# Kernel optimization log

Measured on AMD Instinct MI355X. Metric: run time of the kernel, lower is better.

The kernel has to match this reference:

```python
import jax, jax.numpy as jnp
import numpy as np

B, S, D, H = 4, 2048, 1024, 16
HD = D // H  # head_dim = 64


def setup_inputs() -> dict:
    key = jax.random.key(0)
    ks = jax.random.split(key, 5)
    hidden_states = jax.random.normal(ks[0], (B, S, D), dtype=jnp.float32)
    # GPT-2 Conv1D: out = x @ W + b, W shape [in, out]
    w_attn = jax.random.normal(ks[1], (D, 3 * D), dtype=jnp.float32) * 0.02
    b_attn = jnp.zeros((3 * D,), dtype=jnp.float32)
    w_proj = jax.random.normal(ks[2], (D, D), dtype=jnp.float32) * 0.02
    b_proj = jnp.zeros((D,), dtype=jnp.float32)
    return {"hidden_states": hidden_states, "w_attn": w_attn, "b_attn": b_attn,
            "w_proj": w_proj, "b_proj": b_proj}


def reference(hidden_states, w_attn, b_attn, w_proj, b_proj):
    b, s, d = hidden_states.shape
    qkv = hidden_states @ w_attn + b_attn                     # [B,S,3D]
    q, k, v = jnp.split(qkv, 3, axis=-1)
    # split heads -> [B,H,S,HD]
    def heads(x):
        return x.reshape(b, s, H, HD).transpose(0, 2, 1, 3)
    q, k, v = heads(q), heads(k), heads(v)
    # scaled dot product; GPT-2 divides by sqrt(head_dim)
    scores = jnp.einsum("bhqd,bhkd->bhqk", q, k) / jnp.sqrt(jnp.float32(HD))
    causal = jnp.tril(jnp.ones((s, s), dtype=bool))           # [S,S]
    neg = jnp.finfo(scores.dtype).min
    scores = jnp.where(causal[None, None, :, :], scores, neg)
    attn = jax.nn.softmax(scores, axis=-1)
    ctx = jnp.einsum("bhqk,bhkd->bhqd", attn, v)              # [B,H,S,HD]
    ctx = ctx.transpose(0, 2, 1, 3).reshape(b, s, d)          # merge heads
    return ctx @ w_proj + b_proj
```

## Files before the change

kernel.cpp:

```cpp
#include <hip/hip_runtime.h>
#include <hip/hip_bf16.h>

typedef __bf16 bf16;
typedef bf16 bf16x8 __attribute__((ext_vector_type(8)));
typedef bf16 bf16x4 __attribute__((ext_vector_type(4)));
typedef float f32x4 __attribute__((ext_vector_type(4)));
typedef float f32x16 __attribute__((ext_vector_type(16)));
typedef unsigned int uint2v __attribute__((ext_vector_type(2)));

#define MFMA16(a, b, c) __builtin_amdgcn_mfma_f32_16x16x32_bf16(a, b, c, 0, 0, 0)
#define MFMA32(a, b, c) __builtin_amdgcn_mfma_f32_32x32x16_bf16(a, b, c, 0, 0, 0)

constexpr int Bn = 4, Sn = 2048, Dn = 1024, Hn = 16, HDn = 64;
constexpr int Mn = Bn * Sn;

__device__ __forceinline__ bf16x8 cvt8(float4 a, float4 b) {
  bf16x8 v = {(bf16)a.x, (bf16)a.y, (bf16)a.z, (bf16)a.w,
              (bf16)b.x, (bf16)b.y, (bf16)b.z, (bf16)b.w};
  return v;
}

__device__ __forceinline__ void load_lds16(const bf16* g, bf16* l) {
  __builtin_amdgcn_global_load_lds(
      (const __attribute__((address_space(1))) void*)g,
      (__attribute__((address_space(3))) void*)l, 16, 0, 0);
}

__device__ __forceinline__ unsigned cvt_pk_bf16(float lo, float hi) {
  unsigned r;
  asm("v_cvt_pk_bf16_f32 %0, %1, %2" : "=v"(r) : "v"(lo), "v"(hi));
  return r;
}

__global__ __launch_bounds__(256) void k_prep(const float* __restrict__ hidden,
                                              const float* __restrict__ w_attn,
                                              const float* __restrict__ w_proj,
                                              bf16* __restrict__ Xb,
                                              bf16* __restrict__ wattnT,
                                              bf16* __restrict__ wprojT) {
  __shared__ alignas(16) bf16 t[64][72];
  const int bx = blockIdx.x;
  const int tid = threadIdx.x;
  if (bx < 4096) {
    int i = bx * 256 + tid;
    const float4* p = (const float4*)hidden + (size_t)i * 2;
    float4 a = p[0], b = p[1];
    *((bf16x8*)Xb + i) = cvt8(a, b);
    return;
  }
  const float* in;
  bf16* out;
  int K = 1024, N, n0, k0;
  if (bx < 4864) {
    int idx = bx - 4096;
    in = w_attn; out = wattnT; N = 3072;
    n0 = (idx % 48) * 64; k0 = (idx / 48) * 64;
  } else {
    int idx = bx - 4864;
    in = w_proj; out = wprojT; N = 1024;
    n0 = (idx % 16) * 64; k0 = (idx / 16) * 64;
  }
  {
    int row = tid >> 2;
    int c16 = (tid & 3) * 16;
    const float* src = in + (size_t)(k0 + row) * N + n0 + c16;
    float4 f0 = ((const float4*)src)[0];
    float4 f1 = ((const float4*)src)[1];
    float4 f2 = ((const float4*)src)[2];
    float4 f3 = ((const float4*)src)[3];
    *(bf16x8*)&t[row][c16] = cvt8(f0, f1);
    *(bf16x8*)&t[row][c16 + 8] = cvt8(f2, f3);
  }
  __syncthreads();
#pragma unroll
  for (int i = 0; i < 2; i++) {
    int c = tid + i * 256;
    int nrow = c >> 3, kcol8 = (c & 7) * 8;
    bf16x8 v;
#pragma unroll
    for (int j = 0; j < 8; j++) v[j] = t[kcol8 + j][nrow];
    *(bf16x8*)(out + (size_t)(n0 + nrow) * K + k0 + kcol8) = v;
  }
}


__global__ __launch_bounds__(256) void k_gemm_qkv(const bf16* __restrict__ A,
                                                  const bf16* __restrict__ BT,
                                                  const float* __restrict__ bias,
                                                  bf16* __restrict__ Qo,
                                                  bf16* __restrict__ Ko,
                                                  bf16* __restrict__ Vt) {
  __shared__ alignas(16) bf16 la[128 * 32];
  __shared__ alignas(16) bf16 lb[128 * 32];
  const int tid = threadIdx.x;
  const int w = tid >> 6, lane = tid & 63, l15 = lane & 15, quad = lane >> 4;
  const int wm = w >> 1, wn = w & 1;
  const int bid = blockIdx.x;
  const int xcd = bid & 7, idx = bid >> 3;
  const int by = xcd * 8 + idx / 24;
  const int bx = idx % 24;
  const int m0 = by * 128, n0 = bx * 128;
  const int lrow = lane >> 2, lcol = (lane & 3) * 8;

  f32x4 acc[4][4];
#pragma unroll
  for (int i = 0; i < 4; i++)
#pragma unroll
    for (int j = 0; j < 4; j++) acc[i][j] = f32x4{0.f, 0.f, 0.f, 0.f};

  for (int k0 = 0; k0 < 1024; k0 += 32) {
    __syncthreads();
    load_lds16(A + (size_t)(m0 + w * 16 + lrow) * 1024 + k0 + lcol, &la[w * 512]);
    load_lds16(A + (size_t)(m0 + 64 + w * 16 + lrow) * 1024 + k0 + lcol, &la[(w + 4) * 512]);
    load_lds16(BT + (size_t)(n0 + w * 16 + lrow) * 1024 + k0 + lcol, &lb[w * 512]);
    load_lds16(BT + (size_t)(n0 + 64 + w * 16 + lrow) * 1024 + k0 + lcol, &lb[(w + 4) * 512]);
    __syncthreads();
    bf16x8 af[4], bfr[4];
#pragma unroll
    for (int i = 0; i < 4; i++)
      af[i] = *(const bf16x8*)&la[(wm * 64 + i * 16 + l15) * 32 + quad * 8];
#pragma unroll
    for (int j = 0; j < 4; j++)
      bfr[j] = *(const bf16x8*)&lb[(wn * 64 + j * 16 + l15) * 32 + quad * 8];
#pragma unroll
    for (int i = 0; i < 4; i++)
#pragma unroll
      for (int j = 0; j < 4; j++) acc[i][j] = MFMA16(af[i], bfr[j], acc[i][j]);
  }

#pragma unroll
  for (int j = 0; j < 4; j++) {
    int ng = n0 + wn * 64 + j * 16 + l15;
    float bs = bias[ng];
    int which = ng >> 10;
    int nloc = ng & 1023, hh = nloc >> 6, hd = nloc & 63;
#pragma unroll
    for (int i = 0; i < 4; i++) {
      int mg0 = m0 + wm * 64 + i * 16 + quad * 4;
      int bb = mg0 >> 11, ss = mg0 & 2047;
      if (which == 2) {
        bf16x4 v;
#pragma unroll
        for (int r = 0; r < 4; r++) v[r] = (bf16)(acc[i][j][r] + bs);
        *(bf16x4*)&Vt[((size_t)(bb * Hn + hh) * HDn + hd) * Sn + ss] = v;
      } else {
        bf16* dst = which ? Ko : Qo;
#pragma unroll
        for (int r = 0; r < 4; r++)
          dst[((size_t)(bb * Hn + hh) * Sn + ss + r) * HDn + hd] =
              (bf16)(acc[i][j][r] + bs);
      }
    }
  }
}

__global__ __launch_bounds__(256) void k_gemm_proj(const bf16* __restrict__ A,
                                                   const bf16* __restrict__ BT,
                                                   const float* __restrict__ bias,
                                                   float* __restrict__ out) {
  __shared__ alignas(16) bf16 la[128 * 32];
  __shared__ alignas(16) bf16 lb[128 * 32];
  const int tid = threadIdx.x;
  const int w = tid >> 6, lane = tid & 63, l15 = lane & 15, quad = lane >> 4;
  const int wm = w >> 1, wn = w & 1;
  const int bid = blockIdx.x;
  const int xcd = bid & 7, idx = bid >> 3;
  const int by = xcd * 8 + (idx >> 3);
  const int bx = idx & 7;
  const int m0 = by * 128, n0 = bx * 128;
  const int lrow = lane >> 2, lcol = (lane & 3) * 8;

  f32x4 acc[4][4];
#pragma unroll
  for (int i = 0; i < 4; i++)
#pragma unroll
    for (int j = 0; j < 4; j++) acc[i][j] = f32x4{0.f, 0.f, 0.f, 0.f};

  for (int k0 = 0; k0 < 1024; k0 += 32) {
    __syncthreads();
    load_lds16(A + (size_t)(m0 + w * 16 + lrow) * 1024 + k0 + lcol, &la[w * 512]);
    load_lds16(A + (size_t)(m0 + 64 + w * 16 + lrow) * 1024 + k0 + lcol, &la[(w + 4) * 512]);
    load_lds16(BT + (size_t)(n0 + w * 16 + lrow) * 1024 + k0 + lcol, &lb[w * 512]);
    load_lds16(BT + (size_t)(n0 + 64 + w * 16 + lrow) * 1024 + k0 + lcol, &lb[(w + 4) * 512]);
    __syncthreads();
    bf16x8 af[4], bfr[4];
#pragma unroll
    for (int i = 0; i < 4; i++)
      af[i] = *(const bf16x8*)&la[(wm * 64 + i * 16 + l15) * 32 + quad * 8];
#pragma unroll
    for (int j = 0; j < 4; j++)
      bfr[j] = *(const bf16x8*)&lb[(wn * 64 + j * 16 + l15) * 32 + quad * 8];
#pragma unroll
    for (int i = 0; i < 4; i++)
#pragma unroll
      for (int j = 0; j < 4; j++) acc[i][j] = MFMA16(af[i], bfr[j], acc[i][j]);
  }

#pragma unroll
  for (int j = 0; j < 4; j++) {
    int ng = n0 + wn * 64 + j * 16 + l15;
    float bs = bias[ng];
#pragma unroll
    for (int i = 0; i < 4; i++) {
      int mg0 = m0 + wm * 64 + i * 16 + quad * 4;
#pragma unroll
      for (int r = 0; r < 4; r++)
        out[(size_t)(mg0 + r) * 1024 + ng] = acc[i][j][r] + bs;
    }
  }
}

__global__ __launch_bounds__(256) void k_attn(const bf16* __restrict__ Q,
                                              const bf16* __restrict__ Kv,
                                              const bf16* __restrict__ Vtg,
                                              bf16* __restrict__ ctx) {
  __shared__ alignas(16) bf16 kl[3][64 * 64];
  __shared__ alignas(16) bf16 vl[3][64 * 64];

  const int bh = blockIdx.x;
  const int qt = 15 - blockIdx.y;
  const int bb = bh >> 4, hh = bh & 15;
  const int tid = threadIdx.x;
  const int w = tid >> 6, lane = tid & 63, l31 = lane & 31, hi = lane >> 5;
  const size_t base = (size_t)bh * Sn * HDn;
  const int q0 = qt * 128 + w * 32;
  const int nt = 2 * qt + 2;

  const int r0 = tid >> 3, s0 = tid & 7;
  const int ksw = (s0 ^ (r0 & 7)) << 3;
  const bf16* Krow = Kv + base + (size_t)r0 * 64 + ksw;
  const bf16* Vrow0 = Vtg + ((size_t)bh * 64 + r0) * Sn + ksw;
  const bf16* Vrow1 = Vtg + ((size_t)bh * 64 + r0 + 32) * Sn + ksw;
  const int sw7 = l31 & 7;

  bf16x8 qf[4];
#pragma unroll
  for (int c = 0; c < 4; c++) {
    bf16x8 v = *(const bf16x8*)(Q + base + (size_t)(q0 + l31) * 64 + c * 16 + hi * 8);
#pragma unroll
    for (int e = 0; e < 8; e++) v[e] = (bf16)((float)v[e] * 0.125f);
    qf[c] = v;
  }

  f32x16 o0, o1;
#pragma unroll
  for (int e = 0; e < 16; e++) { o0[e] = 0.f; o1[e] = 0.f; }
  float dsum = 0.f;

#define STAGE(t_, bf_)                                                  \
  {                                                                     \
    const int kb_ = (t_) * 64;                                          \
    load_lds16(Krow + (size_t)kb_ * 64, &kl[bf_][w * 512]);             \
    load_lds16(Krow + (size_t)(kb_ + 32) * 64, &kl[bf_][2048 + w * 512]); \
    load_lds16(Vrow0 + kb_, &vl[bf_][w * 512]);                         \
    load_lds16(Vrow1 + kb_, &vl[bf_][2048 + w * 512]);                  \
  }

  STAGE(0, 0)
  STAGE(1, 1)

  int cb = 0, sb = 2;
  for (int t = 0; t < nt; ++t) {
    if (t == nt - 1) asm volatile("s_waitcnt vmcnt(0)" ::: "memory");
    else             asm volatile("s_waitcnt vmcnt(4)" ::: "memory");
    __builtin_amdgcn_s_barrier();
    if (t + 2 < nt) STAGE(t + 2, sb)
    const int kb = t * 64;
    if (kb <= q0 + 31) {
      const bf16* klc = kl[cb];
      const bf16* vlc = vl[cb];
#pragma unroll
      for (int sub = 0; sub < 2; sub++) {
        const int ks0 = kb + sub * 32;
        if (ks0 > q0 + 31) break;
        f32x16 st;
#pragma unroll
        for (int e = 0; e < 16; e++) st[e] = 0.f;
#pragma unroll
        for (int c = 0; c < 4; c++) {
          const int row = sub * 32 + l31;
          bf16x8 kf = *(const bf16x8*)&klc[row * 64 + (((2 * c + hi) ^ sw7) << 3)];
          st = MFMA32(kf, qf[c], st);
        }
        if (ks0 == q0) {
#pragma unroll
          for (int r = 0; r < 16; r++) {
            int krel = (r & 3) + 8 * (r >> 2) + 4 * hi;
            if (krel > l31) st[r] = -1e30f;
          }
        }
#pragma unroll
        for (int r = 0; r < 16; r++) {
          st[r] = __expf(st[r]);
          dsum += st[r];
        }
#pragma unroll
        for (int c2 = 0; c2 < 2; c2++) {
          unsigned wa0 = cvt_pk_bf16(st[8 * c2 + 0], st[8 * c2 + 1]);
          unsigned wa1 = cvt_pk_bf16(st[8 * c2 + 2], st[8 * c2 + 3]);
          unsigned wb0 = cvt_pk_bf16(st[8 * c2 + 4], st[8 * c2 + 5]);
          unsigned wb1 = cvt_pk_bf16(st[8 * c2 + 6], st[8 * c2 + 7]);
          unsigned pw0, pw1, pw2, pw3;
#if __has_builtin(__builtin_amdgcn_permlane32_swap)
          uint2v sw0 = __builtin_amdgcn_permlane32_swap(wa0, wb0, false, false);
          uint2v sw1 = __builtin_amdgcn_permlane32_swap(wa1, wb1, false, false);
          pw0 = sw0.x; pw1 = sw1.x; pw2 = sw0.y; pw3 = sw1.y;
#else
          unsigned xa0 = __shfl_xor((int)wa0, 32, 64), xb0 = __shfl_xor((int)wb0, 32, 64);
          unsigned xa1 = __shfl_xor((int)wa1, 32, 64), xb1 = __shfl_xor((int)wb1, 32, 64);
          pw0 = hi ? xb0 : wa0; pw1 = hi ? xb1 : wa1;
          pw2 = hi ? wb0 : xa0; pw3 = hi ? wb1 : xa1;
#endif
          union { unsigned u[4]; bf16x8 v; } pb;
          pb.u[0] = pw0; pb.u[1] = pw1; pb.u[2] = pw2; pb.u[3] = pw3;
          const int vs = sub * 4 + 2 * c2;
          bf16x8 vf0 = *(const bf16x8*)&vlc[l31 * 64 + (((vs + hi) ^ sw7) << 3)];
          o0 = MFMA32(vf0, pb.v, o0);
          bf16x8 vf1 = *(const bf16x8*)&vlc[(32 + l31) * 64 + (((vs + hi) ^ sw7) << 3)];
          o1 = MFMA32(vf1, pb.v, o1);
        }
      }
    }
    cb = (cb == 2) ? 0 : cb + 1;
    sb = (sb == 2) ? 0 : sb + 1;
  }
#undef STAGE

  float tot = dsum + __shfl_xor(dsum, 32, 64);
  float inv = 1.f / fmaxf(tot, 1e-20f);
  size_t ob = ((size_t)(bb * Sn + q0 + l31)) * Dn + hh * HDn + hi * 4;
#pragma unroll
  for (int g = 0; g < 4; g++) {
    bf16x4 v0, v1;
#pragma unroll
    for (int r = 0; r < 4; r++) {
      v0[r] = (bf16)(o0[4 * g + r] * inv);
      v1[r] = (bf16)(o1[4 * g + r] * inv);
    }
    *(bf16x4*)&ctx[ob + g * 8] = v0;
    *(bf16x4*)&ctx[ob + 32 + g * 8] = v1;
  }
}

extern "C" void kernel_launch(void* const* d_in, const int* in_sizes, int n_in,
                              void* d_out, int out_size, void* d_ws, size_t ws_size,
                              hipStream_t stream) {
  const float* hidden = (const float*)d_in[0];
  const float* w_attn = (const float*)d_in[1];
  const float* b_attn = (const float*)d_in[2];
  const float* w_proj = (const float*)d_in[3];
  const float* b_proj = (const float*)d_in[4];
  float* out = (float*)d_out;

  bf16* ws = (bf16*)d_ws;
  const size_t QKV_ELEMS = (size_t)Bn * Hn * Sn * HDn;
  bf16* Qb = ws;
  bf16* Kb = Qb + QKV_ELEMS;
  bf16* Vt = Kb + QKV_ELEMS;
  bf16* ctx = Vt + QKV_ELEMS;
  bf16* Xb = ctx;
  bf16* wattnT = ctx + (size_t)Mn * Dn;
  bf16* wprojT = wattnT + (size_t)Dn * 3 * Dn;

  k_prep<<<5120, 256, 0, stream>>>(hidden, w_attn, w_proj, Xb, wattnT, wprojT);
  k_gemm_qkv<<<dim3(1536), 256, 0, stream>>>(Xb, wattnT, b_attn, Qb, Kb, Vt);
  k_attn<<<dim3(64, 16), 256, 0, stream>>>(Qb, Kb, Vt, ctx);
  k_gemm_proj<<<dim3(512), 256, 0, stream>>>(ctx, wprojT, b_proj, out);
}
```

Before: 240.7 us.

## Fuse all four stages into one persistent kernel with grid barriers

Replaces the four separate launches (prep, QKV GEMM, attention, projection GEMM) with a single persistent kernel of 512 blocks. Stages are separated by atomic-counter grid barriers, and each stage loops over its original work units. Attention work is paired so each block handles one heavy and one light query tile (u and 1023-u) to balance the causal load. This removes launch gaps and tail effects, but relies on all 512 blocks being co-resident, adds barrier spin costs, and caps occupancy at the shared 48KB LDS footprint and launch bounds.

```diff
diff --git a/kernel.cpp b/kernel.cpp
--- a/kernel.cpp
+++ b/kernel.cpp
@@ -13,6 +13,7 @@
 
 constexpr int Bn = 4, Sn = 2048, Dn = 1024, Hn = 16, HDn = 64;
 constexpr int Mn = Bn * Sn;
+constexpr unsigned GRID = 512;
 
 __device__ __forceinline__ bf16x8 cvt8(float4 a, float4 b) {
   bf16x8 v = {(bf16)a.x, (bf16)a.y, (bf16)a.z, (bf16)a.w,
@@ -32,313 +33,330 @@
   return r;
 }
 
-__global__ __launch_bounds__(256) void k_prep(const float* __restrict__ hidden,
-                                              const float* __restrict__ w_attn,
-                                              const float* __restrict__ w_proj,
-                                              bf16* __restrict__ Xb,
-                                              bf16* __restrict__ wattnT,
-                                              bf16* __restrict__ wprojT) {
-  __shared__ alignas(16) bf16 t[64][72];
-  const int bx = blockIdx.x;
-  const int tid = threadIdx.x;
-  if (bx < 4096) {
-    int i = bx * 256 + tid;
-    const float4* p = (const float4*)hidden + (size_t)i * 2;
-    float4 a = p[0], b = p[1];
-    *((bf16x8*)Xb + i) = cvt8(a, b);
-    return;
-  }
-  const float* in;
-  bf16* out;
-  int K = 1024, N, n0, k0;
-  if (bx < 4864) {
-    int idx = bx - 4096;
-    in = w_attn; out = wattnT; N = 3072;
-    n0 = (idx % 48) * 64; k0 = (idx / 48) * 64;
-  } else {
-    int idx = bx - 4864;
-    in = w_proj; out = wprojT; N = 1024;
-    n0 = (idx % 16) * 64; k0 = (idx / 16) * 64;
-  }
-  {
-    int row = tid >> 2;
-    int c16 = (tid & 3) * 16;
-    const float* src = in + (size_t)(k0 + row) * N + n0 + c16;
-    float4 f0 = ((const float4*)src)[0];
-    float4 f1 = ((const float4*)src)[1];
-    float4 f2 = ((const float4*)src)[2];
-    float4 f3 = ((const float4*)src)[3];
-    *(bf16x8*)&t[row][c16] = cvt8(f0, f1);
-    *(bf16x8*)&t[row][c16 + 8] = cvt8(f2, f3);
-  }
+__device__ __forceinline__ void grid_barrier(unsigned* ctr) {
   __syncthreads();
-#pragma unroll
-  for (int i = 0; i < 2; i++) {
-    int c = tid + i * 256;
-    int nrow = c >> 3, kcol8 = (c & 7) * 8;
-    bf16x8 v;
-#pragma unroll
-    for (int j = 0; j < 8; j++) v[j] = t[kcol8 + j][nrow];
-    *(bf16x8*)(out + (size_t)(n0 + nrow) * K + k0 + kcol8) = v;
-  }
-}
-
-
-__global__ __launch_bounds__(256) void k_gemm_qkv(const bf16* __restrict__ A,
-                                                  const bf16* __restrict__ BT,
-                                                  const float* __restrict__ bias,
-                                                  bf16* __restrict__ Qo,
-                                                  bf16* __restrict__ Ko,
-                                                  bf16* __restrict__ Vt) {
-  __shared__ alignas(16) bf16 la[128 * 32];
-  __shared__ alignas(16) bf16 lb[128 * 32];
+  __threadfence();
+  if (threadIdx.x == 0) {
+    atomicAdd(ctr, 1u);
+    unsigned tries = 0;
+    while (atomicAdd(ctr, 0u) < GRID) {
+      __builtin_amdgcn_s_sleep(32);
+      if (++tries > 100000000u) break;
+    }
+  }
+  __syncthreads();
+  __threadfence();
+}
+
+__global__ __launch_bounds__(256, 2) void k_fused(
+    const float* __restrict__ hidden, const float* __restrict__ w_attn,
+    const float* __restrict__ w_proj, const float* __restrict__ b_attn,
+    const float* __restrict__ b_proj, bf16* __restrict__ Xb,
+    bf16* __restrict__ wattnT, bf16* __restrict__ wprojT,
+    bf16* __restrict__ Qb, bf16* __restrict__ Kb, bf16* __restrict__ Vt,
+    bf16* __restrict__ ctx, float* __restrict__ out, unsigned* ctrs) {
+  __shared__ alignas(16) unsigned char smem[49152];
+  const int b = blockIdx.x;
   const int tid = threadIdx.x;
   const int w = tid >> 6, lane = tid & 63, l15 = lane & 15, quad = lane >> 4;
-  const int wm = w >> 1, wn = w & 1;
-  const int bid = blockIdx.x;
-  const int xcd = bid & 7, idx = bid >> 3;
-  const int by = xcd * 8 + idx / 24;
-  const int bx = idx % 24;
-  const int m0 = by * 128, n0 = bx * 128;
-  const int lrow = lane >> 2, lcol = (lane & 3) * 8;
-
-  f32x4 acc[4][4];
-#pragma unroll
-  for (int i = 0; i < 4; i++)
-#pragma unroll
-    for (int j = 0; j < 4; j++) acc[i][j] = f32x4{0.f, 0.f, 0.f, 0.f};
-
-  for (int k0 = 0; k0 < 1024; k0 += 32) {
-    __syncthreads();
-    load_lds16(A + (size_t)(m0 + w * 16 + lrow) * 1024 + k0 + lcol, &la[w * 512]);
-    load_lds16(A + (size_t)(m0 + 64 + w * 16 + lrow) * 1024 + k0 + lcol, &la[(w + 4) * 512]);
-    load_lds16(BT + (size_t)(n0 + w * 16 + lrow) * 1024 + k0 + lcol, &lb[w * 512]);
-    load_lds16(BT + (size_t)(n0 + 64 + w * 16 + lrow) * 1024 + k0 + lcol, &lb[(w + 4) * 512]);
-    __syncthreads();
-    bf16x8 af[4], bfr[4];
+
+  {
+    bf16(*t)[72] = (bf16(*)[72])smem;
+    for (int u = b; u < 5120; u += 512) {
+      if (u < 4096) {
+        int i = u * 256 + tid;
+        const float4* p = (const float4*)hidden + (size_t)i * 2;
+        float4 a = p[0], bb = p[1];
+        *((bf16x8*)Xb + i) = cvt8(a, bb);
+      } else {
+        const float* in;
+        bf16* outp;
+        int K = 1024, N, n0, k0;
+        if (u < 4864) {
+          int idx = u - 4096;
+          in = w_attn; outp = wattnT; N = 3072;
+          n0 = (idx % 48) * 64; k0 = (idx / 48) * 64;
+        } else {
+          int idx = u - 4864;
+          in = w_proj; outp = wprojT; N = 1024;
+          n0 = (idx % 16) * 64; k0 = (idx / 16) * 64;
+        }
+        {
+          int row = tid >> 2;
+          int c16 = (tid & 3) * 16;
+          const float* src = in + (size_t)(k0 + row) * N + n0 + c16;
+          float4 f0 = ((const float4*)src)[0];
+          float4 f1 = ((const float4*)src)[1];
+          float4 f2 = ((const float4*)src)[2];
+          float4 f3 = ((const float4*)src)[3];
+          *(bf16x8*)&t[row][c16] = cvt8(f0, f1);
+          *(bf16x8*)&t[row][c16 + 8] = cvt8(f2, f3);
+        }
+        __syncthreads();
+#pragma unroll
+        for (int i = 0; i < 2; i++) {
+          int c = tid + i * 256;
+          int nrow = c >> 3, kcol8 = (c & 7) * 8;
+          bf16x8 v;
+#pragma unroll
+          for (int j = 0; j < 8; j++) v[j] = t[kcol8 + j][nrow];
+          *(bf16x8*)(outp + (size_t)(n0 + nrow) * K + k0 + kcol8) = v;
+        }
+        __syncthreads();
+      }
+    }
+  }
+  grid_barrier(ctrs + 0);
+
+  {
+    bf16* la = (bf16*)smem;
+    bf16* lb = (bf16*)(smem + 8192);
+    const int wm = w >> 1, wn = w & 1;
+    const int lrow = lane >> 2, lcol = (lane & 3) * 8;
+    for (int u = b; u < 1536; u += 512) {
+      const int xcd = u & 7, idx = u >> 3;
+      const int by = xcd * 8 + idx / 24;
+      const int bx = idx % 24;
+      const int m0 = by * 128, n0 = bx * 128;
+
+      f32x4 acc[4][4];
+#pragma unroll
+      for (int i = 0; i < 4; i++)
+#pragma unroll
+        for (int j = 0; j < 4; j++) acc[i][j] = f32x4{0.f, 0.f, 0.f, 0.f};
+
+      for (int k0 = 0; k0 < 1024; k0 += 32) {
+        __syncthreads();
+        load_lds16(Xb + (size_t)(m0 + w * 16 + lrow) * 1024 + k0 + lcol, &la[w * 512]);
+        load_lds16(Xb + (size_t)(m0 + 64 + w * 16 + lrow) * 1024 + k0 + lcol, &la[(w + 4) * 512]);
+        load_lds16(wattnT + (size_t)(n0 + w * 16 + lrow) * 1024 + k0 + lcol, &lb[w * 512]);
+        load_lds16(wattnT + (size_t)(n0 + 64 + w * 16 + lrow) * 1024 + k0 + lcol, &lb[(w + 4) * 512]);
+        __syncthreads();
+        bf16x8 af[4], bfr[4];
+#pragma unroll
+        for (int i = 0; i < 4; i++)
+          af[i] = *(const bf16x8*)&la[(wm * 64 + i * 16 + l15) * 32 + quad * 8];
+#pragma unroll
+        for (int j = 0; j < 4; j++)
+          bfr[j] = *(const bf16x8*)&lb[(wn * 64 + j * 16 + l15) * 32 + quad * 8];
+#pragma unroll
+        for (int i = 0; i < 4; i++)
+#pragma unroll
+          for (int j = 0; j < 4; j++) acc[i][j] = MFMA16(af[i], bfr[j], acc[i][j]);
+      }
+
+#pragma unroll
+      for (int j = 0; j < 4; j++) {
+        int ng = n0 + wn * 64 + j * 16 + l15;
+        float bs = b_attn[ng];
+        int which = ng >> 10;
+        int nloc = ng & 1023, hh = nloc >> 6, hd = nloc & 63;
+#pragma unroll
+        for (int i = 0; i < 4; i++) {
+          int mg0 = m0 + wm * 64 + i * 16 + quad * 4;
+          int bb = mg0 >> 11, ss = mg0 & 2047;
+          if (which == 2) {
+            bf16x4 v;
+#pragma unroll
+            for (int r = 0; r < 4; r++) v[r] = (bf16)(acc[i][j][r] + bs);
+            *(bf16x4*)&Vt[((size_t)(bb * Hn + hh) * HDn + hd) * Sn + ss] = v;
+          } else {
+            bf16* dst = which ? Kb : Qb;
+#pragma unroll
+            for (int r = 0; r < 4; r++)
+              dst[((size_t)(bb * Hn + hh) * Sn + ss + r) * HDn + hd] =
+                  (bf16)(acc[i][j][r] + bs);
+          }
+        }
+      }
+      __syncthreads();
+    }
+  }
+  grid_barrier(ctrs + 1);
+
+  {
+    bf16* kl = (bf16*)smem;
+    bf16* vl = (bf16*)(smem + 24576);
+    const int l31 = lane & 31, hi = lane >> 5;
+    const int r0 = tid >> 3, s0 = tid & 7;
+    const int ksw = (s0 ^ (r0 & 7)) << 3;
+    const int sw7 = l31 & 7;
+
+#pragma unroll 1
+    for (int half = 0; half < 2; ++half) {
+      const int u = half ? (1023 - b) : b;
+      const int bh = u & 63;
+      const int qt = 15 - (u >> 6);
+      const int bb = bh >> 4, hh = bh & 15;
+      const size_t base = (size_t)bh * Sn * HDn;
+      const int q0 = qt * 128 + w * 32;
+      const int nt = 2 * qt + 2;
+
+      const bf16* Krow = Kb + base + (size_t)r0 * 64 + ksw;
+      const bf16* Vrow0 = Vt + ((size_t)bh * 64 + r0) * Sn + ksw;
+      const bf16* Vrow1 = Vt + ((size_t)bh * 64 + r0 + 32) * Sn + ksw;
+
+      bf16x8 qf[4];
+#pragma unroll
+      for (int c = 0; c < 4; c++) {
+        bf16x8 v = *(const bf16x8*)(Qb + base + (size_t)(q0 + l31) * 64 + c * 16 + hi * 8);
+#pragma unroll
+        for (int e = 0; e < 8; e++) v[e] = (bf16)((float)v[e] * 0.125f);
+        qf[c] = v;
+      }
+
+      f32x16 o0, o1;
+#pragma unroll
+      for (int e = 0; e < 16; e++) { o0[e] = 0.f; o1[e] = 0.f; }
+      float dsum = 0.f;
+
+#define STAGE(t_, bf_)                                                        \
+  {                                                                           \
+    const int kb_ = (t_) * 64;                                                \
+    load_lds16(Krow + (size_t)kb_ * 64, kl + (bf_) * 4096 + w * 512);         \
+    load_lds16(Krow + (size_t)(kb_ + 32) * 64,                                \
+               kl + (bf_) * 4096 + 2048 + w * 512);                           \
+    load_lds16(Vrow0 + kb_, vl + (bf_) * 4096 + w * 512);                     \
+    load_lds16(Vrow1 + kb_, vl + (bf_) * 4096 + 2048 + w * 512);              \
+  }
+
+      STAGE(0, 0)
+      STAGE(1, 1)
+
+      int cb = 0, sb = 2;
+      for (int t = 0; t < nt; ++t) {
+        if (t == nt - 1) asm volatile("s_waitcnt vmcnt(0)" ::: "memory");
+        else             asm volatile("s_waitcnt vmcnt(4)" ::: "memory");
+        __builtin_amdgcn_s_barrier();
+        if (t + 2 < nt) STAGE(t + 2, sb)
+        const int kb = t * 64;
+        if (kb <= q0 + 31) {
+          const bf16* klc = kl + cb * 4096;
+          const bf16* vlc = vl + cb * 4096;
+#pragma unroll
+          for (int sub = 0; sub < 2; sub++) {
+            const int ks0 = kb + sub * 32;
+            if (ks0 > q0 + 31) break;
+            f32x16 st;
+#pragma unroll
+            for (int e = 0; e < 16; e++) st[e] = 0.f;
+#pragma unroll
+            for (int c = 0; c < 4; c++) {
+              const int row = sub * 32 + l31;
+              bf16x8 kf = *(const bf16x8*)&klc[row * 64 + (((2 * c + hi) ^ sw7) << 3)];
+              st = MFMA32(kf, qf[c], st);
+            }
+            if (ks0 == q0) {
+#pragma unroll
+              for (int r = 0; r < 16; r++) {
+                int krel = (r & 3) + 8 * (r >> 2) + 4 * hi;
+                if (krel > l31) st[r] = -1e30f;
+              }
+            }
+#pragma unroll
+            for (int r = 0; r < 16; r++) {
+              st[r] = __expf(st[r]);
+              dsum += st[r];
+            }
+#pragma unroll
+            for (int c2 = 0; c2 < 2; c2++) {
+              unsigned wa0 = cvt_pk_bf16(st[8 * c2 + 0], st[8 * c2 + 1]);
+              unsigned wa1 = cvt_pk_bf16(st[8 * c2 + 2], st[8 * c2 + 3]);
+              unsigned wb0 = cvt_pk_bf16(st[8 * c2 + 4], st[8 * c2 + 5]);
+              unsigned wb1 = cvt_pk_bf16(st[8 * c2 + 6], st[8 * c2 + 7]);
+              unsigned pw0, pw1, pw2, pw3;
+#if __has_builtin(__builtin_amdgcn_permlane32_swap)
+              uint2v sw0 = __builtin_amdgcn_permlane32_swap(wa0, wb0, false, false);
+              uint2v sw1 = __builtin_amdgcn_permlane32_swap(wa1, wb1, false, false);
+              pw0 = sw0.x; pw1 = sw1.x; pw2 = sw0.y; pw3 = sw1.y;
+#else
+              unsigned xa0 = __shfl_xor((int)wa0, 32, 64), xb0 = __shfl_xor((int)wb0, 32, 64);
+              unsigned xa1 = __shfl_xor((int)wa1, 32, 64), xb1 = __shfl_xor((int)wb1, 32, 64);
+              pw0 = hi ? xb0 : wa0; pw1 = hi ? xb1 : wa1;
+              pw2 = hi ? wb0 : xa0; pw3 = hi ? wb1 : xa1;
+#endif
+              union { unsigned uu[4]; bf16x8 v; } pb;
+              pb.uu[0] = pw0; pb.uu[1] = pw1; pb.uu[2] = pw2; pb.uu[3] = pw3;
+              const int vs = sub * 4 + 2 * c2;
+              bf16x8 vf0 = *(const bf16x8*)&vlc[l31 * 64 + (((vs + hi) ^ sw7) << 3)];
+              o0 = MFMA32(vf0, pb.v, o0);
+              bf16x8 vf1 = *(const bf16x8*)&vlc[(32 + l31) * 64 + (((vs + hi) ^ sw7) << 3)];
+              o1 = MFMA32(vf1, pb.v, o1);
+            }
+          }
+        }
+        cb = (cb == 2) ? 0 : cb + 1;
+        sb = (sb == 2) ? 0 : sb + 1;
+      }
+#undef STAGE
+
+      float tot = dsum + __shfl_xor(dsum, 32, 64);
+      float inv = 1.f / fmaxf(tot, 1e-20f);
+      size_t ob = ((size_t)(bb * Sn + q0 + l31)) * Dn + hh * HDn + hi * 4;
+#pragma unroll
+      for (int g = 0; g < 4; g++) {
+        bf16x4 v0, v1;
+#pragma unroll
+        for (int r = 0; r < 4; r++) {
+          v0[r] = (bf16)(o0[4 * g + r] * inv);
+          v1[r] = (bf16)(o1[4 * g + r] * inv);
+        }
+        *(bf16x4*)&ctx[ob + g * 8] = v0;
+        *(bf16x4*)&ctx[ob + 32 + g * 8] = v1;
+      }
+      __syncthreads();
+    }
+  }
+  grid_barrier(ctrs + 2);
+
+  {
+    bf16* la = (bf16*)smem;
+    bf16* lb = (bf16*)(smem + 8192);
+    const int wm = w >> 1, wn = w & 1;
+    const int lrow = lane >> 2, lcol = (lane & 3) * 8;
+    const int xcd = b & 7, idx = b >> 3;
+    const int by = xcd * 8 + (idx >> 3);
+    const int bx = idx & 7;
+    const int m0 = by * 128, n0 = bx * 128;
+
+    f32x4 acc[4][4];
 #pragma unroll
     for (int i = 0; i < 4; i++)
-      af[i] = *(const bf16x8*)&la[(wm * 64 + i * 16 + l15) * 32 + quad * 8];
-#pragma unroll
-    for (int j = 0; j < 4; j++)
-      bfr[j] = *(const bf16x8*)&lb[(wn * 64 + j * 16 + l15) * 32 + quad * 8];
-#pragma unroll
-    for (int i = 0; i < 4; i++)
-#pragma unroll
-      for (int j = 0; j < 4; j++) acc[i][j] = MFMA16(af[i], bfr[j], acc[i][j]);
-  }
-
-#pragma unroll
-  for (int j = 0; j < 4; j++) {
-    int ng = n0 + wn * 64 + j * 16 + l15;
-    float bs = bias[ng];
-    int which = ng >> 10;
-    int nloc = ng & 1023, hh = nloc >> 6, hd = nloc & 63;
-#pragma unroll
-    for (int i = 0; i < 4; i++) {
-      int mg0 = m0 + wm * 64 + i * 16 + quad * 4;
-      int bb = mg0 >> 11, ss = mg0 & 2047;
-      if (which == 2) {
-        bf16x4 v;
-#pragma unroll
-        for (int r = 0; r < 4; r++) v[r] = (bf16)(acc[i][j][r] + bs);
-        *(bf16x4*)&Vt[((size_t)(bb * Hn + hh) * HDn + hd) * Sn + ss] = v;
-      } else {
-        bf16* dst = which ? Ko : Qo;
+#pragma unroll
+      for (int j = 0; j < 4; j++) acc[i][j] = f32x4{0.f, 0.f, 0.f, 0.f};
+
+    for (int k0 = 0; k0 < 1024; k0 += 32) {
+      __syncthreads();
+      load_lds16(ctx + (size_t)(m0 + w * 16 + lrow) * 1024 + k0 + lcol, &la[w * 512]);
+      load_lds16(ctx + (size_t)(m0 + 64 + w * 16 + lrow) * 1024 + k0 + lcol, &la[(w + 4) * 512]);
+      load_lds16(wprojT + (size_t)(n0 + w * 16 + lrow) * 1024 + k0 + lcol, &lb[w * 512]);
+      load_lds16(wprojT + (size_t)(n0 + 64 + w * 16 + lrow) * 1024 + k0 + lcol, &lb[(w + 4) * 512]);
+      __syncthreads();
+      bf16x8 af[4], bfr[4];
+#pragma unroll
+      for (int i = 0; i < 4; i++)
+        af[i] = *(const bf16x8*)&la[(wm * 64 + i * 16 + l15) * 32 + quad * 8];
+#pragma unroll
+      for (int j = 0; j < 4; j++)
+        bfr[j] = *(const bf16x8*)&lb[(wn * 64 + j * 16 + l15) * 32 + quad * 8];
+#pragma unroll
+      for (int i = 0; i < 4; i++)
+#pragma unroll
+        for (int j = 0; j < 4; j++) acc[i][j] = MFMA16(af[i], bfr[j], acc[i][j]);
+    }
+
+#pragma unroll
+    for (int j = 0; j < 4; j++) {
+      int ng = n0 + wn * 64 + j * 16 + l15;
+      float bs = b_proj[ng];
+#pragma unroll
+      for (int i = 0; i < 4; i++) {
+        int mg0 = m0 + wm * 64 + i * 16 + quad * 4;
 #pragma unroll
         for (int r = 0; r < 4; r++)
-          dst[((size_t)(bb * Hn + hh) * Sn + ss + r) * HDn + hd] =
-              (bf16)(acc[i][j][r] + bs);
-      }
-    }
-  }
-}
-
-__global__ __launch_bounds__(256) void k_gemm_proj(const bf16* __restrict__ A,
-                                                   const bf16* __restrict__ BT,
-                                                   const float* __restrict__ bias,
-                                                   float* __restrict__ out) {
-  __shared__ alignas(16) bf16 la[128 * 32];
-  __shared__ alignas(16) bf16 lb[128 * 32];
-  const int tid = threadIdx.x;
-  const int w = tid >> 6, lane = tid & 63, l15 = lane & 15, quad = lane >> 4;
-  const int wm = w >> 1, wn = w & 1;
-  const int bid = blockIdx.x;
-  const int xcd = bid & 7, idx = bid >> 3;
-  const int by = xcd * 8 + (idx >> 3);
-  const int bx = idx & 7;
-  const int m0 = by * 128, n0 = bx * 128;
-  const int lrow = lane >> 2, lcol = (lane & 3) * 8;
-
-  f32x4 acc[4][4];
-#pragma unroll
-  for (int i = 0; i < 4; i++)
-#pragma unroll
-    for (int j = 0; j < 4; j++) acc[i][j] = f32x4{0.f, 0.f, 0.f, 0.f};
-
-  for (int k0 = 0; k0 < 1024; k0 += 32) {
-    __syncthreads();
-    load_lds16(A + (size_t)(m0 + w * 16 + lrow) * 1024 + k0 + lcol, &la[w * 512]);
-    load_lds16(A + (size_t)(m0 + 64 + w * 16 + lrow) * 1024 + k0 + lcol, &la[(w + 4) * 512]);
-    load_lds16(BT + (size_t)(n0 + w * 16 + lrow) * 1024 + k0 + lcol, &lb[w * 512]);
-    load_lds16(BT + (size_t)(n0 + 64 + w * 16 + lrow) * 1024 + k0 + lcol, &lb[(w + 4) * 512]);
-    __syncthreads();
-    bf16x8 af[4], bfr[4];
-#pragma unroll
-    for (int i = 0; i < 4; i++)
-      af[i] = *(const bf16x8*)&la[(wm * 64 + i * 16 + l15) * 32 + quad * 8];
-#pragma unroll
-    for (int j = 0; j < 4; j++)
-      bfr[j] = *(const bf16x8*)&lb[(wn * 64 + j * 16 + l15) * 32 + quad * 8];
-#pragma unroll
-    for (int i = 0; i < 4; i++)
-#pragma unroll
-      for (int j = 0; j < 4; j++) acc[i][j] = MFMA16(af[i], bfr[j], acc[i][j]);
-  }
-
-#pragma unroll
-  for (int j = 0; j < 4; j++) {
-    int ng = n0 + wn * 64 + j * 16 + l15;
-    float bs = bias[ng];
-#pragma unroll
-    for (int i = 0; i < 4; i++) {
-      int mg0 = m0 + wm * 64 + i * 16 + quad * 4;
-#pragma unroll
-      for (int r = 0; r < 4; r++)
-        out[(size_t)(mg0 + r) * 1024 + ng] = acc[i][j][r] + bs;
-    }
-  }
-}
-
-__global__ __launch_bounds__(256) void k_attn(const bf16* __restrict__ Q,
-                                              const bf16* __restrict__ Kv,
-                                              const bf16* __restrict__ Vtg,
-                                              bf16* __restrict__ ctx) {
-  __shared__ alignas(16) bf16 kl[3][64 * 64];
-  __shared__ alignas(16) bf16 vl[3][64 * 64];
-
-  const int bh = blockIdx.x;
-  const int qt = 15 - blockIdx.y;
-  const int bb = bh >> 4, hh = bh & 15;
-  const int tid = threadIdx.x;
-  const int w = tid >> 6, lane = tid & 63, l31 = lane & 31, hi = lane >> 5;
-  const size_t base = (size_t)bh * Sn * HDn;
-  const int q0 = qt * 128 + w * 32;
-  const int nt = 2 * qt + 2;
-
-  const int r0 = tid >> 3, s0 = tid & 7;
-  const int ksw = (s0 ^ (r0 & 7)) << 3;
-  const bf16* Krow = Kv + base + (size_t)r0 * 64 + ksw;
-  const bf16* Vrow0 = Vtg + ((size_t)bh * 64 + r0) * Sn + ksw;
-  const bf16* Vrow1 = Vtg + ((size_t)bh * 64 + r0 + 32) * Sn + ksw;
-  const int sw7 = l31 & 7;
-
-  bf16x8 qf[4];
-#pragma unroll
-  for (int c = 0; c < 4; c++) {
-    bf16x8 v = *(const bf16x8*)(Q + base + (size_t)(q0 + l31) * 64 + c * 16 + hi * 8);
-#pragma unroll
-    for (int e = 0; e < 8; e++) v[e] = (bf16)((float)v[e] * 0.125f);
-    qf[c] = v;
-  }
-
-  f32x16 o0, o1;
-#pragma unroll
-  for (int e = 0; e < 16; e++) { o0[e] = 0.f; o1[e] = 0.f; }
-  float dsum = 0.f;
-
-#define STAGE(t_, bf_)                                                  \
-  {                                                                     \
-    const int kb_ = (t_) * 64;                                          \
-    load_lds16(Krow + (size_t)kb_ * 64, &kl[bf_][w * 512]);             \
-    load_lds16(Krow + (size_t)(kb_ + 32) * 64, &kl[bf_][2048 + w * 512]); \
-    load_lds16(Vrow0 + kb_, &vl[bf_][w * 512]);                         \
-    load_lds16(Vrow1 + kb_, &vl[bf_][2048 + w * 512]);                  \
-  }
-
-  STAGE(0, 0)
-  STAGE(1, 1)
-
-  int cb = 0, sb = 2;
-  for (int t = 0; t < nt; ++t) {
-    if (t == nt - 1) asm volatile("s_waitcnt vmcnt(0)" ::: "memory");
-    else             asm volatile("s_waitcnt vmcnt(4)" ::: "memory");
-    __builtin_amdgcn_s_barrier();
-    if (t + 2 < nt) STAGE(t + 2, sb)
-    const int kb = t * 64;
-    if (kb <= q0 + 31) {
-      const bf16* klc = kl[cb];
-      const bf16* vlc = vl[cb];
-#pragma unroll
-      for (int sub = 0; sub < 2; sub++) {
-        const int ks0 = kb + sub * 32;
-        if (ks0 > q0 + 31) break;
-        f32x16 st;
-#pragma unroll
-        for (int e = 0; e < 16; e++) st[e] = 0.f;
-#pragma unroll
-        for (int c = 0; c < 4; c++) {
-          const int row = sub * 32 + l31;
-          bf16x8 kf = *(const bf16x8*)&klc[row * 64 + (((2 * c + hi) ^ sw7) << 3)];
-          st = MFMA32(kf, qf[c], st);
-        }
-        if (ks0 == q0) {
-#pragma unroll
-          for (int r = 0; r < 16; r++) {
-            int krel = (r & 3) + 8 * (r >> 2) + 4 * hi;
-            if (krel > l31) st[r] = -1e30f;
-          }
-        }
-#pragma unroll
-        for (int r = 0; r < 16; r++) {
-          st[r] = __expf(st[r]);
-          dsum += st[r];
-        }
-#pragma unroll
-        for (int c2 = 0; c2 < 2; c2++) {
-          unsigned wa0 = cvt_pk_bf16(st[8 * c2 + 0], st[8 * c2 + 1]);
-          unsigned wa1 = cvt_pk_bf16(st[8 * c2 + 2], st[8 * c2 + 3]);
-          unsigned wb0 = cvt_pk_bf16(st[8 * c2 + 4], st[8 * c2 + 5]);
-          unsigned wb1 = cvt_pk_bf16(st[8 * c2 + 6], st[8 * c2 + 7]);
-          unsigned pw0, pw1, pw2, pw3;
-#if __has_builtin(__builtin_amdgcn_permlane32_swap)
-          uint2v sw0 = __builtin_amdgcn_permlane32_swap(wa0, wb0, false, false);
-          uint2v sw1 = __builtin_amdgcn_permlane32_swap(wa1, wb1, false, false);
-          pw0 = sw0.x; pw1 = sw1.x; pw2 = sw0.y; pw3 = sw1.y;
-#else
-          unsigned xa0 = __shfl_xor((int)wa0, 32, 64), xb0 = __shfl_xor((int)wb0, 32, 64);
-          unsigned xa1 = __shfl_xor((int)wa1, 32, 64), xb1 = __shfl_xor((int)wb1, 32, 64);
-          pw0 = hi ? xb0 : wa0; pw1 = hi ? xb1 : wa1;
-          pw2 = hi ? wb0 : xa0; pw3 = hi ? wb1 : xa1;
-#endif
-          union { unsigned u[4]; bf16x8 v; } pb;
-          pb.u[0] = pw0; pb.u[1] = pw1; pb.u[2] = pw2; pb.u[3] = pw3;
-          const int vs = sub * 4 + 2 * c2;
-          bf16x8 vf0 = *(const bf16x8*)&vlc[l31 * 64 + (((vs + hi) ^ sw7) << 3)];
-          o0 = MFMA32(vf0, pb.v, o0);
-          bf16x8 vf1 = *(const bf16x8*)&vlc[(32 + l31) * 64 + (((vs + hi) ^ sw7) << 3)];
-          o1 = MFMA32(vf1, pb.v, o1);
-        }
-      }
-    }
-    cb = (cb == 2) ? 0 : cb + 1;
-    sb = (sb == 2) ? 0 : sb + 1;
-  }
-#undef STAGE
-
-  float tot = dsum + __shfl_xor(dsum, 32, 64);
-  float inv = 1.f / fmaxf(tot, 1e-20f);
-  size_t ob = ((size_t)(bb * Sn + q0 + l31)) * Dn + hh * HDn + hi * 4;
-#pragma unroll
-  for (int g = 0; g < 4; g++) {
-    bf16x4 v0, v1;
-#pragma unroll
-    for (int r = 0; r < 4; r++) {
-      v0[r] = (bf16)(o0[4 * g + r] * inv);
-      v1[r] = (bf16)(o1[4 * g + r] * inv);
-    }
-    *(bf16x4*)&ctx[ob + g * 8] = v0;
-    *(bf16x4*)&ctx[ob + 32 + g * 8] = v1;
+          out[(size_t)(mg0 + r) * 1024 + ng] = acc[i][j][r] + bs;
+      }
+    }
   }
 }
 
@@ -361,9 +379,10 @@
   bf16* Xb = ctx;
   bf16* wattnT = ctx + (size_t)Mn * Dn;
   bf16* wprojT = wattnT + (size_t)Dn * 3 * Dn;
-
-  k_prep<<<5120, 256, 0, stream>>>(hidden, w_attn, w_proj, Xb, wattnT, wprojT);
-  k_gemm_qkv<<<dim3(1536), 256, 0, stream>>>(Xb, wattnT, b_attn, Qb, Kb, Vt);
-  k_attn<<<dim3(64, 16), 256, 0, stream>>>(Qb, Kb, Vt, ctx);
-  k_gemm_proj<<<dim3(512), 256, 0, stream>>>(ctx, wprojT, b_proj, out);
-}
+  unsigned* ctrs = (unsigned*)(wprojT + (size_t)Dn * Dn);
+
+  hipMemsetAsync(ctrs, 0, 3 * sizeof(unsigned), stream);
+  k_fused<<<dim3(GRID), dim3(256), 0, stream>>>(
+      hidden, w_attn, w_proj, b_attn, b_proj, Xb, wattnT, wprojT, Qb, Kb, Vt,
+      ctx, out, ctrs);
+}
```

Result: slower. 592.7 us (+146.2%).
